# Performance work log

Measured on AMD Instinct MI355X. Metric: run time of the kernel, lower is better.

Reference implementation:

```python
import jax, jax.numpy as jnp
import numpy as np

V, E, U = 32000, 256, 512  # vocab, embed dim, LSTM units
B, S = 16, 130             # batch, seq len


def lstm_layer(x, mask, k, r, b):
    """Keras LSTMCell semantics. x:[B,T,D], mask:[B,T]; gates order i,f,c,o."""
    h0 = jnp.zeros((x.shape[0], U), x.dtype)
    c0 = h0
    xs = jnp.swapaxes(x, 0, 1)      # [T,B,D]
    ms = jnp.swapaxes(mask, 0, 1)   # [T,B]

    def step(carry, inp):
        h, c = carry
        xt, mt = inp
        z = xt @ k + h @ r + b
        i, f, g, o = jnp.split(z, 4, axis=-1)
        i = jax.nn.sigmoid(i); f = jax.nn.sigmoid(f); o = jax.nn.sigmoid(o)
        cn = f * c + i * jnp.tanh(g)
        hn = o * jnp.tanh(cn)
        m = mt[:, None]
        hn = jnp.where(m, hn, h)  # masked steps carry previous state/output
        cn = jnp.where(m, cn, c)
        return (hn, cn), hn

    _, ys = jax.lax.scan(step, (h0, c0), (xs, ms))
    return jnp.swapaxes(ys, 0, 1)  # [B,T,U]


def stacked_lstm(x, mask, params):
    h = x
    for (k, r, b) in params:
        h = lstm_layer(h, mask, k, r, b)
    return h


def setup_inputs() -> dict:
    key = jax.random.key(0)
    ks = jax.random.split(key, 20)
    d = {}
    d["seqs"] = jax.random.randint(ks[0], (B, S), 0, V)
    d["emb"] = jax.random.normal(ks[1], (V, E), jnp.float32) * 0.01
    i = 2
    for pre in ("f", "b"):
        in_dims = [E, U]
        for l in range(2):
            d[f"{pre}k{l}"] = jax.random.normal(ks[i], (in_dims[l], 4 * U), jnp.float32) * 0.05; i += 1
            d[f"{pre}r{l}"] = jax.random.normal(ks[i], (U, 4 * U), jnp.float32) * 0.05; i += 1
            d[f"{pre}b{l}"] = jnp.zeros((4 * U,), jnp.float32)
    d["Wp"] = jax.random.normal(ks[i], (2 * U, V), jnp.float32) * 0.02
    d["bp"] = jnp.zeros((V,), jnp.float32)
    return d


def reference(seqs, emb, fk0, fr0, fb0, fk1, fr1, fb1, bk0, br0, bb0, bk1, br1, bb1, Wp, bp):
    mask = seqs != 0                 # mask_zero=True
    embedded = emb[seqs]             # [B,S,E]
    # forward LM over tokens 0..S-2
    f = stacked_lstm(embedded[:, :-1], mask[:, :-1], [(fk0, fr0, fb0), (fk1, fr1, fb1)])
    # backward LM over tokens 1..S-1 (go_backwards: scan reversed input)
    xb = embedded[:, 1:][:, ::-1]
    mb = mask[:, 1:][:, ::-1]
    b = stacked_lstm(xb, mb, [(bk0, br0, bb0), (bk1, br1, bb1)])
    b_rev = b[:, ::-1]               # tf.reverse -> chronological order
    o = jnp.concatenate([f[:, :-1], b_rev[:, 1:]], axis=-1)  # [B,S-2,2U]
    return o @ Wp + bp               # [B,S-2,V]
```

## Files before the change

### kernel.cpp

```cpp
#include <hip/hip_runtime.h>

typedef __attribute__((ext_vector_type(8))) short bf16x8;
typedef __attribute__((ext_vector_type(4))) float f32x4;

__device__ __forceinline__ unsigned short f2bf(float x){
  union { float f; unsigned u; } v; v.f = x;
  unsigned r = v.u + 0x7FFFu + ((v.u >> 16) & 1u);
  return (unsigned short)(r >> 16);
}

#define BYPASS_ST_SHORT(base, val) \
  asm volatile("global_store_short %0, %1, off sc0 sc1" :: "v"(base), "v"(val))

__device__ __forceinline__ int ld_flag(const int* p){
  int v;
  asm volatile("global_load_dword %0, %1, off sc0 sc1\n\t"
               "s_waitcnt vmcnt(0)"
               : "=v"(v) : "v"(p) : "memory");
  return v;
}

__device__ __forceinline__ void gload_lds16(const void* g, void* l){
  __builtin_amdgcn_global_load_lds(
      (const __attribute__((address_space(1))) unsigned*)g,
      (__attribute__((address_space(3))) unsigned*)l, 16, 0, 0);
}

__global__ void embed_kernel(const int* __restrict__ seqs, const float* __restrict__ emb,
                             unsigned short* __restrict__ x, int* __restrict__ mask,
                             int* __restrict__ flags){
  const int t = blockIdx.x, b = blockIdx.y, l = threadIdx.x;
  if (t == 0 && b == 0){
    #pragma unroll
    for (int j = 0; j < 16; ++j) flags[l + j*64] = 0;
  }
  const int tok = seqs[b*130 + t];
  if (l == 0) mask[b*130 + t] = (tok != 0) ? 1 : 0;
  const float* src = emb + (size_t)tok * 256;
  unsigned short* dst = x + ((size_t)b*130 + t)*256;
  #pragma unroll
  for (int j = 0; j < 4; ++j) dst[l + j*64] = f2bf(src[l + j*64]);
}

__global__ void transpose_bf16(const float* __restrict__ in, unsigned short* __restrict__ out,
                               int R, int C){
  __shared__ float tile[32][33];
  const int c0 = blockIdx.x*32, r0 = blockIdx.y*32;
  const int tx = threadIdx.x, ty = threadIdx.y;
  #pragma unroll
  for (int j = 0; j < 32; j += 8) tile[ty+j][tx] = in[(size_t)(r0+ty+j)*C + (c0+tx)];
  __syncthreads();
  #pragma unroll
  for (int j = 0; j < 32; j += 8) out[(size_t)(c0+ty+j)*R + (r0+tx)] = f2bf(tile[tx][ty+j]);
}

__global__ __launch_bounds__(512, 2) void lstm_coop(
    const unsigned short* __restrict__ x, const int* __restrict__ maskg,
    const unsigned short* __restrict__ fk0T, const unsigned short* __restrict__ fr0T,
    const unsigned short* __restrict__ fk1T, const unsigned short* __restrict__ fr1T,
    const unsigned short* __restrict__ bk0T, const unsigned short* __restrict__ br0T,
    const unsigned short* __restrict__ bk1T, const unsigned short* __restrict__ br1T,
    const float* __restrict__ fb0, const float* __restrict__ fb1,
    const float* __restrict__ bb0, const float* __restrict__ bb1,
    unsigned short* h0f, unsigned short* h0b,
    unsigned short* aproj, int* flags)
{
  const int wg = blockIdx.x;
  const int dir = wg >> 5;
  const int layer = (wg >> 4) & 1;
  const int u0 = (wg & 15) * 32;
  const int tid = threadIdx.x;
  const int w = tid >> 6, l = tid & 63;
  const int gate = w >> 1, half = w & 1;
  const int lr = l & 15, lk = l >> 4;
  const int cglob = gate*512 + u0 + half*16 + lr;

  const unsigned short* kT = (layer == 0) ? (dir ? bk0T : fk0T) : (dir ? bk1T : fk1T);
  const unsigned short* rT = (layer == 0) ? (dir ? br0T : fr0T) : (dir ? br1T : fr1T);
  const float* bias = (layer == 0) ? (dir ? bb0 : fb0) : (dir ? bb1 : fb1);
  unsigned short* h0 = dir ? h0b : h0f;

  int* fown  = flags + (layer*2 + dir)*256;
  int* fprod = flags + dir*256;
  int* fself = fown + (wg & 15)*16;

  bf16x8 wreg[16], kreg[16];
  #pragma unroll
  for (int i = 0; i < 16; ++i)
    wreg[i] = *(const bf16x8*)(rT + (size_t)cglob*512 + i*32 + lk*8);
  if (layer == 0){
    #pragma unroll
    for (int i = 0; i < 8; ++i)
      kreg[i] = *(const bf16x8*)(kT + (size_t)cglob*256 + i*32 + lk*8);
  } else {
    #pragma unroll
    for (int i = 0; i < 16; ++i)
      kreg[i] = *(const bf16x8*)(kT + (size_t)cglob*512 + i*32 + lk*8);
  }

  __shared__ float z_lds[4][16][32];
  __shared__ int mask_s[16*130];
  __shared__ __attribute__((aligned(16))) char h_lds[16*1024];
  __shared__ __attribute__((aligned(16))) char h2_lds[16*1024];
  for (int i = tid; i < 16*130; i += 512) mask_s[i] = maskg[i];

  float c_reg = 0.f, h_reg = 0.f;
  const int gu = tid & 31, gb = tid >> 5;
  const float bzi = bias[u0+gu], bzf = bias[512 + u0+gu];
  const float bzc = bias[1024 + u0+gu], bzo = bias[1536 + u0+gu];
  __syncthreads();

  for (int t = 0; t < 128; ++t){
    if (w == 0){
      const int* fp = nullptr; int tgt = 0;
      if (l < 16){ fp = fown + l*16; tgt = t; }
      else if (l < 32 && layer == 1){ fp = fprod + (l-16)*16; tgt = t + 1; }
      if (fp){
        while (ld_flag(fp) < tgt) __builtin_amdgcn_s_sleep(1);
      }
    }
    __syncthreads();

    const int r0s = w*2;
    if (layer == 0){
      if (t > 0){
        #pragma unroll
        for (int j = 0; j < 2; ++j){
          const int r = r0s + j;
          const unsigned short* g = h0 + ((size_t)(t-1)*16 + r)*512 + ((l ^ (r & 7))*8);
          gload_lds16(g, h_lds + r*1024);
        }
      }
    } else {
      #pragma unroll
      for (int j = 0; j < 2; ++j){
        const int r = r0s + j;
        const unsigned short* g = h0 + ((size_t)t*16 + r)*512 + ((l ^ (r & 7))*8);
        gload_lds16(g, h_lds + r*1024);
      }
      if (t > 0){
        const int prow = dir ? (128 - t) : (t - 1);
        #pragma unroll
        for (int j = 0; j < 2; ++j){
          const int r = r0s + j;
          const unsigned short* g = aproj + ((size_t)(r*128 + prow))*1024 + dir*512 + ((l ^ (r & 7))*8);
          gload_lds16(g, h2_lds + r*1024);
        }
      }
    }

    f32x4 acc = {0.f, 0.f, 0.f, 0.f};
    const int fsw = (lr & 7) << 4;
    if (layer == 0){
      const int pos = dir ? (129 - t) : t;
      const unsigned short* xa = x + ((size_t)lr*130 + pos)*256 + lk*8;
      #pragma unroll
      for (int i = 0; i < 8; ++i){
        bf16x8 a = *(const bf16x8*)(xa + i*32);
        acc = __builtin_amdgcn_mfma_f32_16x16x32_bf16(a, kreg[i], acc, 0, 0, 0);
      }
      if (t > 0){
        asm volatile("s_waitcnt vmcnt(0)" ::: "memory");
        __syncthreads();
        #pragma unroll
        for (int i = 0; i < 16; ++i){
          bf16x8 a = *(const bf16x8*)(h_lds + lr*1024 + ((lk*16 + i*64) ^ fsw));
          acc = __builtin_amdgcn_mfma_f32_16x16x32_bf16(a, wreg[i], acc, 0, 0, 0);
        }
      }
    } else {
      asm volatile("s_waitcnt vmcnt(0)" ::: "memory");
      __syncthreads();
      #pragma unroll
      for (int i = 0; i < 16; ++i){
        bf16x8 a = *(const bf16x8*)(h_lds + lr*1024 + ((lk*16 + i*64) ^ fsw));
        acc = __builtin_amdgcn_mfma_f32_16x16x32_bf16(a, kreg[i], acc, 0, 0, 0);
      }
      if (t > 0){
        #pragma unroll
        for (int i = 0; i < 16; ++i){
          bf16x8 a = *(const bf16x8*)(h2_lds + lr*1024 + ((lk*16 + i*64) ^ fsw));
          acc = __builtin_amdgcn_mfma_f32_16x16x32_bf16(a, wreg[i], acc, 0, 0, 0);
        }
      }
    }
    #pragma unroll
    for (int r = 0; r < 4; ++r) z_lds[gate][lk*4 + r][half*16 + lr] = acc[r];
    __syncthreads();

    {
      const float zi = z_lds[0][gb][gu] + bzi;
      const float zf = z_lds[1][gb][gu] + bzf;
      const float zc = z_lds[2][gb][gu] + bzc;
      const float zo = z_lds[3][gb][gu] + bzo;
      const float iv = 1.f / (1.f + expf(-zi));
      const float fv = 1.f / (1.f + expf(-zf));
      const float ov = 1.f / (1.f + expf(-zo));
      const float gv = tanhf(zc);
      float cn = fv*c_reg + iv*gv;
      float hn = ov*tanhf(cn);
      const int pos = dir ? (129 - t) : t;
      if (mask_s[gb*130 + pos] == 0){ cn = c_reg; hn = h_reg; }
      c_reg = cn; h_reg = hn;
      const unsigned short hb = f2bf(hn);
      if (layer == 0){
        unsigned short* p = h0 + ((size_t)t*16 + gb)*512 + u0 + gu;
        BYPASS_ST_SHORT(p, (unsigned)hb);
      } else {
        const int row = dir ? (127 - t) : t;
        unsigned short* p = aproj + ((size_t)gb*128 + row)*1024 + dir*512 + u0 + gu;
        BYPASS_ST_SHORT(p, (unsigned)hb);
      }
    }
    asm volatile("s_waitcnt vmcnt(0)" ::: "memory");
    __syncthreads();
    if (tid == 0){
      int v = t + 1;
      asm volatile("global_store_dword %0, %1, off sc0 sc1" :: "v"(fself), "v"(v) : "memory");
    }
  }
}

__global__ __launch_bounds__(256) void gemm_bf16(
    const unsigned short* __restrict__ A, const unsigned short* __restrict__ Bt,
    const float* __restrict__ bias, float* __restrict__ C,
    int M, int N, int K)
{
  __shared__ unsigned short lA[128*32], lB[128*32];
  const int tid = threadIdx.x;
  const int w = tid >> 6, l = tid & 63;
  const int wr = w >> 1, wc = w & 1;
  const int lr = l & 15, lk = l >> 4;
  const int brow = blockIdx.y * 128, bcol = blockIdx.x * 128;
  f32x4 acc[4][4] = {};
  for (int k0 = 0; k0 < K; k0 += 32){
    __syncthreads();
    #pragma unroll
    for (int j = 0; j < 2; ++j){
      const int base = w*2048 + j*1024;
      const int L = base + l*16;
      const int Lg = L ^ (((L >> 7) & 3) << 4);
      const int row = Lg >> 6, kb = Lg & 63;
      gload_lds16((const char*)(A + (size_t)(brow+row)*K + k0) + kb, (char*)lA + base);
      gload_lds16((const char*)(Bt + (size_t)(bcol+row)*K + k0) + kb, (char*)lB + base);
    }
    __syncthreads();
    bf16x8 af[4], bfr[4];
    #pragma unroll
    for (int m = 0; m < 4; ++m){
      const int L = (wr*64 + m*16 + lr)*64 + lk*16;
      const int sp = L ^ (((L >> 7) & 3) << 4);
      af[m] = *(const bf16x8*)((char*)lA + sp);
    }
    #pragma unroll
    for (int n = 0; n < 4; ++n){
      const int L = (wc*64 + n*16 + lr)*64 + lk*16;
      const int sp = L ^ (((L >> 7) & 3) << 4);
      bfr[n] = *(const bf16x8*)((char*)lB + sp);
    }
    #pragma unroll
    for (int m = 0; m < 4; ++m)
      #pragma unroll
      for (int n = 0; n < 4; ++n)
        acc[m][n] = __builtin_amdgcn_mfma_f32_16x16x32_bf16(af[m], bfr[n], acc[m][n], 0, 0, 0);
  }
  #pragma unroll
  for (int m = 0; m < 4; ++m){
    #pragma unroll
    for (int n = 0; n < 4; ++n){
      const int col = bcol + wc*64 + n*16 + lr;
      const float bv = bias[col];
      const int row0 = brow + wr*64 + m*16 + lk*4;
      #pragma unroll
      for (int r = 0; r < 4; ++r)
        C[(size_t)(row0 + r)*N + col] = acc[m][n][r] + bv;
    }
  }
}

extern "C" void kernel_launch(void* const* d_in, const int* in_sizes, int n_in,
                              void* d_out, int out_size, void* d_ws, size_t ws_size,
                              hipStream_t stream){
  (void)in_sizes; (void)n_in; (void)out_size; (void)ws_size;
  const int*   seqs = (const int*)d_in[0];
  const float* emb  = (const float*)d_in[1];
  const float* fk0  = (const float*)d_in[2];
  const float* fr0  = (const float*)d_in[3];
  const float* fb0  = (const float*)d_in[4];
  const float* fk1  = (const float*)d_in[5];
  const float* fr1  = (const float*)d_in[6];
  const float* fb1  = (const float*)d_in[7];
  const float* bk0  = (const float*)d_in[8];
  const float* br0  = (const float*)d_in[9];
  const float* bb0  = (const float*)d_in[10];
  const float* bk1  = (const float*)d_in[11];
  const float* br1  = (const float*)d_in[12];
  const float* bb1  = (const float*)d_in[13];
  const float* Wp   = (const float*)d_in[14];
  const float* bp   = (const float*)d_in[15];
  float* out = (float*)d_out;

  char* ws = (char*)d_ws;
  size_t off = 0;
  auto alloc = [&](size_t b){ size_t o = off; off += (b + 255) & ~(size_t)255; return o; };
  int* flags            = (int*)(ws + alloc(4096));
  unsigned short* x     = (unsigned short*)(ws + alloc((size_t)16*130*256*2));
  int* mask             = (int*)(ws + alloc((size_t)16*130*4));
  unsigned short* fk0T  = (unsigned short*)(ws + alloc((size_t)2048*256*2));
  unsigned short* fr0T  = (unsigned short*)(ws + alloc((size_t)2048*512*2));
  unsigned short* fk1T  = (unsigned short*)(ws + alloc((size_t)2048*512*2));
  unsigned short* fr1T  = (unsigned short*)(ws + alloc((size_t)2048*512*2));
  unsigned short* bk0T  = (unsigned short*)(ws + alloc((size_t)2048*256*2));
  unsigned short* br0T  = (unsigned short*)(ws + alloc((size_t)2048*512*2));
  unsigned short* bk1T  = (unsigned short*)(ws + alloc((size_t)2048*512*2));
  unsigned short* br1T  = (unsigned short*)(ws + alloc((size_t)2048*512*2));
  unsigned short* h0f   = (unsigned short*)(ws + alloc((size_t)128*16*512*2));
  unsigned short* h0b   = (unsigned short*)(ws + alloc((size_t)128*16*512*2));
  unsigned short* aproj = (unsigned short*)(ws + alloc((size_t)2048*1024*2));
  unsigned short* WpT   = (unsigned short*)(ws + alloc((size_t)32000*1024*2));

  embed_kernel<<<dim3(130,16), 64, 0, stream>>>(seqs, emb, x, mask, flags);

  dim3 tb(32, 8);
  transpose_bf16<<<dim3(64, 8),   tb, 0, stream>>>(fk0, fk0T, 256, 2048);
  transpose_bf16<<<dim3(64, 16),  tb, 0, stream>>>(fr0, fr0T, 512, 2048);
  transpose_bf16<<<dim3(64, 16),  tb, 0, stream>>>(fk1, fk1T, 512, 2048);
  transpose_bf16<<<dim3(64, 16),  tb, 0, stream>>>(fr1, fr1T, 512, 2048);
  transpose_bf16<<<dim3(64, 8),   tb, 0, stream>>>(bk0, bk0T, 256, 2048);
  transpose_bf16<<<dim3(64, 16),  tb, 0, stream>>>(br0, br0T, 512, 2048);
  transpose_bf16<<<dim3(64, 16),  tb, 0, stream>>>(bk1, bk1T, 512, 2048);
  transpose_bf16<<<dim3(64, 16),  tb, 0, stream>>>(br1, br1T, 512, 2048);
  transpose_bf16<<<dim3(1000, 32), tb, 0, stream>>>(Wp, WpT, 1024, 32000);

  lstm_coop<<<64, 512, 0, stream>>>(x, mask,
      fk0T, fr0T, fk1T, fr1T, bk0T, br0T, bk1T, br1T,
      fb0, fb1, bb0, bb1, h0f, h0b, aproj, flags);

  gemm_bf16<<<dim3(250, 16), 256, 0, stream>>>(aproj, WpT, bp, out, 2048, 32000, 1024);
}
```

Baseline: 858.4 us.

## Fuse weight transposes into one persistent kernel and remap GEMM tiles per XCD

Nine separate transpose launches become one grid-stride kernel that handles every weight matrix, using 32x64 tiles and 512 threads, which cuts launch overhead and tail effects. The GEMM moves to a 1D grid whose block index is remapped so consecutive blocks landing on the same XCD (orig & 7) work on neighbouring tiles. All 16 M-tiles that share an N column are grouped together, so each Wp slice is fetched into a single XCD's L2. The risk is that the fixed 256-block grid-stride loop serialises tiles and adds a __syncthreads per tile.

```diff
diff --git a/kernel.cpp b/kernel.cpp
--- a/kernel.cpp
+++ b/kernel.cpp
@@ -42,16 +42,50 @@
   for (int j = 0; j < 4; ++j) dst[l + j*64] = f2bf(src[l + j*64]);
 }
 
-__global__ void transpose_bf16(const float* __restrict__ in, unsigned short* __restrict__ out,
-                               int R, int C){
-  __shared__ float tile[32][33];
-  const int c0 = blockIdx.x*32, r0 = blockIdx.y*32;
-  const int tx = threadIdx.x, ty = threadIdx.y;
-  #pragma unroll
-  for (int j = 0; j < 32; j += 8) tile[ty+j][tx] = in[(size_t)(r0+ty+j)*C + (c0+tx)];
-  __syncthreads();
-  #pragma unroll
-  for (int j = 0; j < 32; j += 8) out[(size_t)(c0+ty+j)*R + (r0+tx)] = f2bf(tile[tx][ty+j]);
+__global__ __launch_bounds__(512) void prep_transpose(
+    const float* __restrict__ Wp,  unsigned short* __restrict__ WpT,
+    const float* __restrict__ fk0, unsigned short* __restrict__ fk0T,
+    const float* __restrict__ fr0, unsigned short* __restrict__ fr0T,
+    const float* __restrict__ fk1, unsigned short* __restrict__ fk1T,
+    const float* __restrict__ fr1, unsigned short* __restrict__ fr1T,
+    const float* __restrict__ bk0, unsigned short* __restrict__ bk0T,
+    const float* __restrict__ br0, unsigned short* __restrict__ br0T,
+    const float* __restrict__ bk1, unsigned short* __restrict__ bk1T,
+    const float* __restrict__ br1, unsigned short* __restrict__ br1T)
+{
+  __shared__ float tf[32*65];
+  const int tid = threadIdx.x;
+  const int tx = tid & 63, ty = tid >> 6;
+  const int orow = tid & 31, oc = tid >> 5;
+  for (int tile = blockIdx.x; tile < 19584; tile += gridDim.x){
+    const float* src; unsigned short* dst; int R, C, r0, c0;
+    if (tile < 16000){
+      src = Wp; dst = WpT; R = 1024; C = 32000;
+      const int kt = tile / 500, nt = tile - kt*500;
+      r0 = kt*32; c0 = nt*64;
+    } else {
+      int u = tile - 16000;
+      C = 2048;
+      if (u < 256)      { src = fk0; dst = fk0T; R = 256;           }
+      else if (u < 768) { src = fr0; dst = fr0T; R = 512; u -= 256; }
+      else if (u < 1280){ src = fk1; dst = fk1T; R = 512; u -= 768; }
+      else if (u < 1792){ src = fr1; dst = fr1T; R = 512; u -= 1280;}
+      else if (u < 2048){ src = bk0; dst = bk0T; R = 256; u -= 1792;}
+      else if (u < 2560){ src = br0; dst = br0T; R = 512; u -= 2048;}
+      else if (u < 3072){ src = bk1; dst = bk1T; R = 512; u -= 2560;}
+      else              { src = br1; dst = br1T; R = 512; u -= 3072;}
+      const int kt = u >> 5, nt = u & 31;
+      r0 = kt*32; c0 = nt*64;
+    }
+    #pragma unroll
+    for (int j = 0; j < 4; ++j)
+      tf[(ty + 8*j)*65 + tx] = src[(size_t)(r0 + ty + 8*j)*C + c0 + tx];
+    __syncthreads();
+    #pragma unroll
+    for (int j = 0; j < 4; ++j)
+      dst[(size_t)(c0 + oc + 16*j)*R + r0 + orow] = f2bf(tf[orow*65 + oc + 16*j]);
+    __syncthreads();
+  }
 }
 
 __global__ __launch_bounds__(512, 2) void lstm_coop(
@@ -231,7 +265,11 @@
   const int w = tid >> 6, l = tid & 63;
   const int wr = w >> 1, wc = w & 1;
   const int lr = l & 15, lk = l >> 4;
-  const int brow = blockIdx.y * 128, bcol = blockIdx.x * 128;
+  const int orig = blockIdx.x;
+  const int logical = (orig & 7)*500 + (orig >> 3);
+  const int mt = logical & 15;
+  const int nt = logical >> 4;
+  const int brow = mt * 128, bcol = nt * 128;
   f32x4 acc[4][4] = {};
   for (int k0 = 0; k0 < K; k0 += 32){
     __syncthreads();
@@ -321,20 +359,13 @@
 
   embed_kernel<<<dim3(130,16), 64, 0, stream>>>(seqs, emb, x, mask, flags);
 
-  dim3 tb(32, 8);
-  transpose_bf16<<<dim3(64, 8),   tb, 0, stream>>>(fk0, fk0T, 256, 2048);
-  transpose_bf16<<<dim3(64, 16),  tb, 0, stream>>>(fr0, fr0T, 512, 2048);
-  transpose_bf16<<<dim3(64, 16),  tb, 0, stream>>>(fk1, fk1T, 512, 2048);
-  transpose_bf16<<<dim3(64, 16),  tb, 0, stream>>>(fr1, fr1T, 512, 2048);
-  transpose_bf16<<<dim3(64, 8),   tb, 0, stream>>>(bk0, bk0T, 256, 2048);
-  transpose_bf16<<<dim3(64, 16),  tb, 0, stream>>>(br0, br0T, 512, 2048);
-  transpose_bf16<<<dim3(64, 16),  tb, 0, stream>>>(bk1, bk1T, 512, 2048);
-  transpose_bf16<<<dim3(64, 16),  tb, 0, stream>>>(br1, br1T, 512, 2048);
-  transpose_bf16<<<dim3(1000, 32), tb, 0, stream>>>(Wp, WpT, 1024, 32000);
+  prep_transpose<<<256, 512, 0, stream>>>(Wp, WpT,
+      fk0, fk0T, fr0, fr0T, fk1, fk1T, fr1, fr1T,
+      bk0, bk0T, br0, br0T, bk1, bk1T, br1, br1T);
 
   lstm_coop<<<64, 512, 0, stream>>>(x, mask,
       fk0T, fr0T, fk1T, fr1T, bk0T, br0T, bk1T, br1T,
       fb0, fb1, bb0, bb1, h0f, h0b, aproj, flags);
 
-  gemm_bf16<<<dim3(250, 16), 256, 0, stream>>>(aproj, WpT, bp, out, 2048, 32000, 1024);
-}
+  gemm_bf16<<<4000, 256, 0, stream>>>(aproj, WpT, bp, out, 2048, 32000, 1024);
+}
```

Measured after the change: 871.7 us. Within noise of the previous version (+1.6%).
